# Kernel tuning notes

Measured on AMD Instinct MI355X. Metric: run time of the kernel, lower is better.

## Reference

```python
import jax, jax.numpy as jnp
import numpy as np

B, IN_F, OUT_F, H = 2048, 512, 512, 8
D = OUT_F // H  # head_dim = 64


def setup_inputs() -> dict:
    key = jax.random.key(0)
    ks = jax.random.split(key, 4)
    x = jax.random.normal(ks[0], (B, IN_F), dtype=jnp.float32)
    # learned params (per init_kwargs): nn.Linear(IN_F, OUT_F) and attention vector a
    W_w = jax.random.normal(ks[1], (OUT_F, IN_F), dtype=jnp.float32) * (1.0 / np.sqrt(IN_F))
    W_b = jnp.zeros((OUT_F,), dtype=jnp.float32)
    a = jax.random.normal(ks[2], (2 * D, 1), dtype=jnp.float32) * 0.1
    adj = jax.random.randint(ks[3], (B, B), 0, 2, dtype=jnp.int32)
    return {"x": x, "adj": adj, "W_w": W_w, "W_b": W_b, "a": a}


def reference(x, adj, W_w, W_b, a):
    Bn = x.shape[0]
    # h: [B, H, D]
    h = (x @ W_w.T + W_b).reshape(Bn, H, D)
    # decompose shared attention vector into src/dst halves (same for every head,
    # since torch code tiles a across heads via a.repeat(1, num_heads))
    a_src, a_dst = a[:D, 0], a[D:, 0]
    s_src = jnp.einsum('bhd,d->bh', h, a_src)  # [B, H] contribution of node i
    s_dst = jnp.einsum('bhd,d->bh', h, a_dst)  # [B, H] contribution of node j
    # e[i, j, h] = leakyrelu(h_i . a_src + h_j . a_dst)  -> [B, B, H]
    e = jax.nn.leaky_relu(s_src[:, None, :] + s_dst[None, :, :], negative_slope=0.2)
    e = jnp.where(adj[:, :, None] == 0, jnp.float32(-1e9), e)
    attn = jax.nn.softmax(e, axis=1)  # softmax over neighbors j (torch dim=1)
    # h_prime[i, h, :] = sum_j attn[i, j, h] * h[j, h, :]
    h_prime = jnp.einsum('ijh,jhd->ihd', attn, h).reshape(Bn, H * D)
    return jax.nn.elu(h_prime)
```

## Files before the change

### kernel.cpp

```cpp
#include <hip/hip_runtime.h>
#include <hip/hip_bf16.h>
#include <math.h>
#include <stdint.h>

#define BN 2048
#define KF 512
#define OF 512
#define NH 8
#define DD 64

typedef __attribute__((ext_vector_type(8))) short short8;
typedef __attribute__((ext_vector_type(4))) float f32x4;
typedef unsigned short ushortT;

static __device__ __forceinline__ ushortT bfcvt(float f) {
  __hip_bfloat16 h = __float2bfloat16(f);
  return *reinterpret_cast<ushortT*>(&h);
}
static __device__ __forceinline__ float bf2f(ushortT b) {
  return __uint_as_float(((unsigned)b) << 16);
}

#define SPLIT8(vsrc, dhi, dlo)                                        \
  {                                                                   \
    ushortT hi8[8], lo8[8];                                           \
    _Pragma("unroll") for (int i = 0; i < 8; ++i) {                   \
      hi8[i] = bfcvt((vsrc)[i]);                                      \
      lo8[i] = bfcvt((vsrc)[i] - bf2f(hi8[i]));                       \
    }                                                                 \
    (dhi) = *(const int4*)hi8;                                        \
    (dlo) = *(const int4*)lo8;                                        \
  }

__global__ __launch_bounds__(256, 2) void k_main(
    const float* __restrict__ x, const int* __restrict__ adj,
    const float* __restrict__ W, const float* __restrict__ Wb,
    const float* __restrict__ av,
    ushortT* __restrict__ hF, float* __restrict__ E12s, float* __restrict__ E12d,
    uint8_t* __restrict__ adjB) {
  __shared__ __align__(16) uint8_t smem[24576];
  __shared__ float sredS[2][32], sredD[2][32];

  const int t    = threadIdx.x;
  const int hh   = blockIdx.x;
  const int i0   = blockIdx.y * 32;
  const int b    = hh * 64 + blockIdx.y;
  const int lane = t & 63;
  const int wv   = t >> 6;
  const int mt   = wv & 1;
  const int nt   = wv >> 1;
  const int l15  = lane & 15;
  const int lq   = lane >> 4;

  {
    const int gtid = b * 256 + t;
#pragma unroll
    for (int it = 0; it < 4; ++it) {
      const int bidx = gtid + it * (512 * 256);
      const int4 v0 = *(const int4*)(adj + (size_t)bidx * 8);
      const int4 v1 = *(const int4*)(adj + (size_t)bidx * 8 + 4);
      unsigned m = (v0.x ? 1u : 0u) | (v0.y ? 2u : 0u) | (v0.z ? 4u : 0u) | (v0.w ? 8u : 0u)
                 | (v1.x ? 16u : 0u) | (v1.y ? 32u : 0u) | (v1.z ? 64u : 0u) | (v1.w ? 128u : 0u);
      adjB[bidx] = (uint8_t)m;
    }
  }

  ushortT* sAh = (ushortT*)smem;
  ushortT* sAl = sAh + 32 * 64;
  ushortT* sBh = sAl + 32 * 64;
  ushortT* sBl = sBh + 64 * 64;

  f32x4 acc[2] = {};
  const int srow = t >> 3, ss = t & 7;
  int4 aHi, aLo, bHi[2], bLo[2];

  {
    const float* xs = x + (size_t)(i0 + srow) * KF + ss * 8;
    float v[8];
    *(float4*)&v[0] = *(const float4*)xs;
    *(float4*)&v[4] = *(const float4*)(xs + 4);
    SPLIT8(v, aHi, aLo)
#pragma unroll
    for (int rp = 0; rp < 2; ++rp) {
      const int S = t + rp * 256, rw = S >> 3, s2 = S & 7;
      const float* wsrc = W + (size_t)(hh * 64 + rw) * KF + s2 * 8;
      float wv8[8];
      *(float4*)&wv8[0] = *(const float4*)wsrc;
      *(float4*)&wv8[4] = *(const float4*)(wsrc + 4);
      SPLIT8(wv8, bHi[rp], bLo[rp])
    }
  }

  for (int k0 = 0; k0 < 8; ++k0) {
    __syncthreads();
    {
      const int offA = srow * 64 + ((ss ^ (srow & 7)) * 8);
      *(int4*)&sAh[offA] = aHi;
      *(int4*)&sAl[offA] = aLo;
#pragma unroll
      for (int rp = 0; rp < 2; ++rp) {
        const int S = t + rp * 256, rw = S >> 3, s2 = S & 7;
        const int offB = rw * 64 + ((s2 ^ (rw & 7)) * 8);
        *(int4*)&sBh[offB] = bHi[rp];
        *(int4*)&sBl[offB] = bLo[rp];
      }
    }
    __syncthreads();
    if (k0 < 7) {
      const int kc = (k0 + 1) * 64;
      const float* xs = x + (size_t)(i0 + srow) * KF + kc + ss * 8;
      float v[8];
      *(float4*)&v[0] = *(const float4*)xs;
      *(float4*)&v[4] = *(const float4*)(xs + 4);
      SPLIT8(v, aHi, aLo)
#pragma unroll
      for (int rp = 0; rp < 2; ++rp) {
        const int S = t + rp * 256, rw = S >> 3, s2 = S & 7;
        const float* wsrc = W + (size_t)(hh * 64 + rw) * KF + kc + s2 * 8;
        float wv8[8];
        *(float4*)&wv8[0] = *(const float4*)wsrc;
        *(float4*)&wv8[4] = *(const float4*)(wsrc + 4);
        SPLIT8(wv8, bHi[rp], bLo[rp])
      }
    }
#pragma unroll
    for (int kb = 0; kb < 2; ++kb) {
      const int sc = kb * 4 + lq;
      const int arow = mt * 16 + l15;
      const int offA = arow * 64 + ((sc ^ (arow & 7)) * 8);
      const short8 afh = *(const short8*)&sAh[offA];
      const short8 afl = *(const short8*)&sAl[offA];
      const int br0 = nt * 32 + l15;
      const int br1 = br0 + 16;
      const int offB0 = br0 * 64 + ((sc ^ (br0 & 7)) * 8);
      const int offB1 = br1 * 64 + ((sc ^ (br1 & 7)) * 8);
      const short8 bh0 = *(const short8*)&sBh[offB0];
      const short8 bl0 = *(const short8*)&sBl[offB0];
      const short8 bh1 = *(const short8*)&sBh[offB1];
      const short8 bl1 = *(const short8*)&sBl[offB1];
      acc[0] = __builtin_amdgcn_mfma_f32_16x16x32_bf16(afh, bh0, acc[0], 0, 0, 0);
      acc[1] = __builtin_amdgcn_mfma_f32_16x16x32_bf16(afh, bh1, acc[1], 0, 0, 0);
      acc[0] = __builtin_amdgcn_mfma_f32_16x16x32_bf16(afh, bl0, acc[0], 0, 0, 0);
      acc[1] = __builtin_amdgcn_mfma_f32_16x16x32_bf16(afh, bl1, acc[1], 0, 0, 0);
      acc[0] = __builtin_amdgcn_mfma_f32_16x16x32_bf16(afl, bh0, acc[0], 0, 0, 0);
      acc[1] = __builtin_amdgcn_mfma_f32_16x16x32_bf16(afl, bh1, acc[1], 0, 0, 0);
    }
  }

  __syncthreads();
  ushortT* ldsT = (ushortT*)smem;
  float bias2[2], asv[2], adv[2];
#pragma unroll
  for (int bb = 0; bb < 2; ++bb) {
    const int fl = nt * 32 + bb * 16 + l15;
    bias2[bb] = Wb[hh * 64 + fl];
    asv[bb] = av[fl];
    adv[bb] = av[DD + fl];
  }
#pragma unroll
  for (int p = 0; p < 4; ++p) {
    float vs = 0.f, vd = 0.f;
#pragma unroll
    for (int bb = 0; bb < 2; ++bb) {
      const float hv = acc[bb][p] + bias2[bb];
      const ushortT hu = bfcvt(hv);
      vs = fmaf(hv, asv[bb], vs);
      vd = fmaf(hv, adv[bb], vd);
      ldsT[(nt * 32 + bb * 16 + l15) * 40 + mt * 16 + lq * 4 + p] = hu;
    }
    vs += __shfl_xor(vs, 1); vs += __shfl_xor(vs, 2);
    vs += __shfl_xor(vs, 4); vs += __shfl_xor(vs, 8);
    vd += __shfl_xor(vd, 1); vd += __shfl_xor(vd, 2);
    vd += __shfl_xor(vd, 4); vd += __shfl_xor(vd, 8);
    if (l15 == 0) {
      sredS[nt][mt * 16 + lq * 4 + p] = vs;
      sredD[nt][mt * 16 + lq * 4 + p] = vd;
    }
  }
  __syncthreads();
  if (t < 32) {
    const float s1 = sredS[0][t] + sredS[1][t];
    const float s2 = sredD[0][t] + sredD[1][t];
    const size_t gi = (size_t)hh * BN + i0 + t;
    float2 sv; sv.x = __expf(s1); sv.y = __expf(0.2f * s1);
    float2 dv; dv.x = __expf(s2); dv.y = __expf(0.2f * s2);
    *(float2*)&E12s[gi * 2] = sv;
    *(float2*)&E12d[gi * 2] = dv;
  }
  {
    const int n = t >> 6, ln = t & 63;
    const int4 v = *(const int4*)&ldsT[(n * 16 + (ln & 15)) * 40 + ((ln >> 4) * 8)];
    const size_t chunk = (((size_t)hh * 64 + blockIdx.y) * 4 + n) * 64 + ln;
    *(int4*)&hF[chunk * 8] = v;
  }
}

__global__ __launch_bounds__(512, 4) void k_attn(
    const ushortT* __restrict__ hF, const uint8_t* __restrict__ adjB,
    const float* __restrict__ E12s, const float* __restrict__ E12d,
    float* __restrict__ out) {
  __shared__ __align__(16) float e12[BN * 2];
  __shared__ __align__(16) float cbuf[4][2 * 16 * 68];
  __shared__ uint8_t abits[32 * 272];
  __shared__ float denP[8][2][16];
  __shared__ unsigned mlut[4];

  const int t    = threadIdx.x;
  const int hh   = blockIdx.x;
  const int i0   = blockIdx.y * 32;
  const int lane = t & 63;
  const int wv   = t >> 6;
  const int l15  = lane & 15;
  const int lq   = lane >> 4;

  {
    const float4* g = (const float4*)(E12d + (size_t)hh * BN * 2);
    ((float4*)e12)[t]       = g[t];
    ((float4*)e12)[t + 512] = g[t + 512];
    const int r = t >> 4, pp = t & 15;
    *(int4*)(abits + r * 272 + pp * 16) =
        *(const int4*)(adjB + (size_t)(i0 + r) * 256 + pp * 16);
    if (t < 4) mlut[t] = (t & 1 ? 0x0000FFFFu : 0u) | (t & 2 ? 0xFFFF0000u : 0u);
  }

  const float2 eiA = *(const float2*)&E12s[2 * ((size_t)hh * BN + i0 + l15)];
  const float2 eiB = *(const float2*)&E12s[2 * ((size_t)hh * BN + i0 + 16 + l15)];

  f32x4 acc0[4] = {};
  f32x4 acc1[4] = {};
  f32x4 accd0 = {0.f, 0.f, 0.f, 0.f}, accd1 = {0.f, 0.f, 0.f, 0.f};

  const short8 ones8 = {(short)0x3F80, (short)0x3F80, (short)0x3F80, (short)0x3F80,
                        (short)0x3F80, (short)0x3F80, (short)0x3F80, (short)0x3F80};

  const ushortT* hfb = hF + (size_t)hh * 64 * 4 * 64 * 8 + (size_t)lane * 8;

  __syncthreads();

  const int c0 = wv * 4;
  for (int c = c0; c < c0 + 4; ++c) {
    const uint64_t bits0 = *(const uint64_t*)(abits + l15 * 272 + c * 8);
    const uint64_t bits1 = *(const uint64_t*)(abits + (16 + l15) * 272 + c * 8);
#pragma unroll
    for (int kb = 0; kb < 2; ++kb) {
      const int jb = c * 2 + kb;
      const int j0 = jb * 32 + lq * 8;
      const float* ep = &e12[j0 * 2];
      const float4 r0 = *(const float4*)(ep);
      const float4 r1 = *(const float4*)(ep + 4);
      const float4 r2 = *(const float4*)(ep + 8);
      const float4 r3 = *(const float4*)(ep + 12);
      const unsigned bb0 = (unsigned)(bits0 >> ((kb * 4 + lq) * 8)) & 0xffu;
      const unsigned bb1 = (unsigned)(bits1 >> ((kb * 4 + lq) * 8)) & 0xffu;
      unsigned pk0[4], pk1[4];
#pragma unroll
      for (int q = 0; q < 4; ++q) {
        const float4 rq = (q == 0) ? r0 : (q == 1) ? r1 : (q == 2) ? r2 : r3;
        const float d1a = rq.x, d2a = rq.y, d1b = rq.z, d2b = rq.w;
        const unsigned m0 = mlut[(bb0 >> (2 * q)) & 3u];
        const unsigned m1 = mlut[(bb1 >> (2 * q)) & 3u];
        const float wa0 = fmaxf(eiA.x * d1a, eiA.y * d2a);
        const float wb0 = fmaxf(eiA.x * d1b, eiA.y * d2b);
        pk0[q] = (((unsigned)bfcvt(wa0)) | (((unsigned)bfcvt(wb0)) << 16)) & m0;
        const float wa1 = fmaxf(eiB.x * d1a, eiB.y * d2a);
        const float wb1 = fmaxf(eiB.x * d1b, eiB.y * d2b);
        pk1[q] = (((unsigned)bfcvt(wa1)) | (((unsigned)bfcvt(wb1)) << 16)) & m1;
      }
      const short8 af0 = *(const short8*)pk0;
      const short8 af1 = *(const short8*)pk1;
      const ushortT* fb = hfb + (size_t)(jb * 4) * 64 * 8;
#pragma unroll
      for (int n = 0; n < 4; ++n) {
        const short8 bf = *(const short8*)(fb + (size_t)n * 64 * 8);
        acc0[n] = __builtin_amdgcn_mfma_f32_16x16x32_bf16(af0, bf, acc0[n], 0, 0, 0);
        acc1[n] = __builtin_amdgcn_mfma_f32_16x16x32_bf16(af1, bf, acc1[n], 0, 0, 0);
      }
      accd0 = __builtin_amdgcn_mfma_f32_16x16x32_bf16(af0, ones8, accd0, 0, 0, 0);
      accd1 = __builtin_amdgcn_mfma_f32_16x16x32_bf16(af1, ones8, accd1, 0, 0, 0);
    }
  }

  if (l15 == 0) {
#pragma unroll
    for (int p = 0; p < 4; ++p) {
      denP[wv][0][lq * 4 + p] = accd0[p];
      denP[wv][1][lq * 4 + p] = accd1[p];
    }
  }

#define CWRITE(buf)                                                     \
  _Pragma("unroll") for (int n = 0; n < 4; ++n)                         \
  _Pragma("unroll") for (int p = 0; p < 4; ++p) {                       \
    (buf)[(lq * 4 + p) * 68 + n * 16 + l15]      = acc0[n][p];          \
    (buf)[(16 + lq * 4 + p) * 68 + n * 16 + l15] = acc1[n][p];          \
  }
#define CADD(buf)                                                       \
  _Pragma("unroll") for (int n = 0; n < 4; ++n)                         \
  _Pragma("unroll") for (int p = 0; p < 4; ++p) {                       \
    acc0[n][p] += (buf)[(lq * 4 + p) * 68 + n * 16 + l15];              \
    acc1[n][p] += (buf)[(16 + lq * 4 + p) * 68 + n * 16 + l15];         \
  }

  if (wv >= 4) { CWRITE(cbuf[wv - 4]) }
  __syncthreads();
  if (wv < 4) {
    CADD(cbuf[wv])
    if (wv >= 2) { CWRITE(cbuf[wv]) }
  }
  __syncthreads();
  if (wv < 2) {
    CADD(cbuf[wv + 2])
    if (wv == 1) { CWRITE(cbuf[1]) }
  }
  __syncthreads();
  if (wv == 0) {
    CADD(cbuf[1])
    float dfin0[4], dfin1[4];
#pragma unroll
    for (int p = 0; p < 4; ++p) {
      const int row = lq * 4 + p;
      float d0 = 0.f, d1s = 0.f;
#pragma unroll
      for (int w = 0; w < 8; ++w) { d0 += denP[w][0][row]; d1s += denP[w][1][row]; }
      dfin0[p] = 1.f / d0;
      dfin1[p] = 1.f / d1s;
    }
#pragma unroll
    for (int n = 0; n < 4; ++n)
#pragma unroll
      for (int p = 0; p < 4; ++p) {
        float v0 = acc0[n][p] * dfin0[p];
        float v1 = acc1[n][p] * dfin1[p];
        v0 = v0 > 0.f ? v0 : expm1f(v0);
        v1 = v1 > 0.f ? v1 : expm1f(v1);
        out[(size_t)(i0 + lq * 4 + p) * OF + hh * 64 + n * 16 + l15] = v0;
        out[(size_t)(i0 + 16 + lq * 4 + p) * OF + hh * 64 + n * 16 + l15] = v1;
      }
  }
#undef CWRITE
#undef CADD
}

extern "C" void kernel_launch(void* const* d_in, const int* in_sizes, int n_in,
                              void* d_out, int out_size, void* d_ws, size_t ws_size,
                              hipStream_t stream) {
  const float* x  = (const float*)d_in[0];
  const int* adj  = (const int*)d_in[1];
  const float* Ww = (const float*)d_in[2];
  const float* Wb = (const float*)d_in[3];
  const float* a  = (const float*)d_in[4];
  float* outp = (float*)d_out;

  uint8_t* p = (uint8_t*)d_ws;
  ushortT* hF   = (ushortT*)(p + 0x000000);
  float*   E12d = (float*)  (p + 0x200000);
  float*   E12s = (float*)  (p + 0x220000);
  uint8_t* adjB =            p + 0x240000;

  k_main<<<dim3(NH, BN / 32), 256, 0, stream>>>(x, adj, Ww, Wb, a, hF, E12s, E12d, adjB);
  k_attn<<<dim3(NH, BN / 32), 512, 0, stream>>>(hF, adjB, E12s, E12d, outp);
}
```

Measured before the change: 34.34 us.

## Fully unroll attention loop with double-buffered B loads and packed bf16 conversion

Fully unrolls the eight per-wave j-blocks and double-buffers the global hF fragment loads, so the next block's B operands are requested while the current block's MFMAs run. Adjacency bits are loaded once per wave as uint4 words. The shared-memory mask lookup table is replaced by per-element selects, and bf16 packing uses the v_cvt_pk_bf16_f32 instruction. The aim is to hide global load latency and cut LDS and ALU work, at the cost of more registers, which may reduce occupancy.

Result: faster. 33.06 us, median of 2 (-3.7%).

```diff
diff --git a/kernel.cpp b/kernel.cpp
--- a/kernel.cpp
+++ b/kernel.cpp
@@ -203,7 +203,6 @@
   __shared__ __align__(16) float cbuf[4][2 * 16 * 68];
   __shared__ uint8_t abits[32 * 272];
   __shared__ float denP[8][2][16];
-  __shared__ unsigned mlut[4];
 
   const int t    = threadIdx.x;
   const int hh   = blockIdx.x;
@@ -220,65 +219,84 @@
     const int r = t >> 4, pp = t & 15;
     *(int4*)(abits + r * 272 + pp * 16) =
         *(const int4*)(adjB + (size_t)(i0 + r) * 256 + pp * 16);
-    if (t < 4) mlut[t] = (t & 1 ? 0x0000FFFFu : 0u) | (t & 2 ? 0xFFFF0000u : 0u);
   }
 
   const float2 eiA = *(const float2*)&E12s[2 * ((size_t)hh * BN + i0 + l15)];
   const float2 eiB = *(const float2*)&E12s[2 * ((size_t)hh * BN + i0 + 16 + l15)];
 
-  f32x4 acc0[4] = {};
-  f32x4 acc1[4] = {};
-  f32x4 accd0 = {0.f, 0.f, 0.f, 0.f}, accd1 = {0.f, 0.f, 0.f, 0.f};
-
   const short8 ones8 = {(short)0x3F80, (short)0x3F80, (short)0x3F80, (short)0x3F80,
                         (short)0x3F80, (short)0x3F80, (short)0x3F80, (short)0x3F80};
 
-  const ushortT* hfb = hF + (size_t)hh * 64 * 4 * 64 * 8 + (size_t)lane * 8;
-
-  __syncthreads();
-
-  const int c0 = wv * 4;
-  for (int c = c0; c < c0 + 4; ++c) {
-    const uint64_t bits0 = *(const uint64_t*)(abits + l15 * 272 + c * 8);
-    const uint64_t bits1 = *(const uint64_t*)(abits + (16 + l15) * 272 + c * 8);
-#pragma unroll
-    for (int kb = 0; kb < 2; ++kb) {
-      const int jb = c * 2 + kb;
-      const int j0 = jb * 32 + lq * 8;
-      const float* ep = &e12[j0 * 2];
-      const float4 r0 = *(const float4*)(ep);
-      const float4 r1 = *(const float4*)(ep + 4);
-      const float4 r2 = *(const float4*)(ep + 8);
-      const float4 r3 = *(const float4*)(ep + 12);
-      const unsigned bb0 = (unsigned)(bits0 >> ((kb * 4 + lq) * 8)) & 0xffu;
-      const unsigned bb1 = (unsigned)(bits1 >> ((kb * 4 + lq) * 8)) & 0xffu;
-      unsigned pk0[4], pk1[4];
-#pragma unroll
-      for (int q = 0; q < 4; ++q) {
-        const float4 rq = (q == 0) ? r0 : (q == 1) ? r1 : (q == 2) ? r2 : r3;
-        const float d1a = rq.x, d2a = rq.y, d1b = rq.z, d2b = rq.w;
-        const unsigned m0 = mlut[(bb0 >> (2 * q)) & 3u];
-        const unsigned m1 = mlut[(bb1 >> (2 * q)) & 3u];
-        const float wa0 = fmaxf(eiA.x * d1a, eiA.y * d2a);
-        const float wb0 = fmaxf(eiA.x * d1b, eiA.y * d2b);
-        pk0[q] = (((unsigned)bfcvt(wa0)) | (((unsigned)bfcvt(wb0)) << 16)) & m0;
-        const float wa1 = fmaxf(eiB.x * d1a, eiB.y * d2a);
-        const float wb1 = fmaxf(eiB.x * d1b, eiB.y * d2b);
-        pk1[q] = (((unsigned)bfcvt(wa1)) | (((unsigned)bfcvt(wb1)) << 16)) & m1;
-      }
-      const short8 af0 = *(const short8*)pk0;
-      const short8 af1 = *(const short8*)pk1;
-      const ushortT* fb = hfb + (size_t)(jb * 4) * 64 * 8;
-#pragma unroll
-      for (int n = 0; n < 4; ++n) {
-        const short8 bf = *(const short8*)(fb + (size_t)n * 64 * 8);
-        acc0[n] = __builtin_amdgcn_mfma_f32_16x16x32_bf16(af0, bf, acc0[n], 0, 0, 0);
-        acc1[n] = __builtin_amdgcn_mfma_f32_16x16x32_bf16(af1, bf, acc1[n], 0, 0, 0);
-      }
-      accd0 = __builtin_amdgcn_mfma_f32_16x16x32_bf16(af0, ones8, accd0, 0, 0, 0);
-      accd1 = __builtin_amdgcn_mfma_f32_16x16x32_bf16(af1, ones8, accd1, 0, 0, 0);
-    }
-  }
+  const ushortT* hfb = hF + (size_t)hh * 131072 + (size_t)lane * 8;
+
+  __syncthreads();
+
+  const uint4 wA0 = *(const uint4*)(abits + l15 * 272 + wv * 32);
+  const uint4 wA1 = *(const uint4*)(abits + l15 * 272 + wv * 32 + 16);
+  const uint4 wB0 = *(const uint4*)(abits + (16 + l15) * 272 + wv * 32);
+  const uint4 wB1 = *(const uint4*)(abits + (16 + l15) * 272 + wv * 32 + 16);
+  const int lqs = lq * 8;
+
+  f32x4 acc0[4] = {}, acc1[4] = {};
+  f32x4 accd0 = {0.f, 0.f, 0.f, 0.f}, accd1 = {0.f, 0.f, 0.f, 0.f};
+
+  const int jb0 = wv * 8;
+  short8 bfA[4], bfB[4];
+  {
+    const ushortT* b0 = hfb + (size_t)(jb0 * 4) * 512;
+#pragma unroll
+    for (int n = 0; n < 4; ++n) bfA[n] = *(const short8*)(b0 + (size_t)n * 512);
+  }
+
+#define WSEL0(s) ((s)==0?wA0.x:(s)==1?wA0.y:(s)==2?wA0.z:(s)==3?wA0.w: \
+                  (s)==4?wA1.x:(s)==5?wA1.y:(s)==6?wA1.z:wA1.w)
+#define WSEL1(s) ((s)==0?wB0.x:(s)==1?wB0.y:(s)==2?wB0.z:(s)==3?wB0.w: \
+                  (s)==4?wB1.x:(s)==5?wB1.y:(s)==6?wB1.z:wB1.w)
+
+#define STEP(s, BCUR, BNXT)                                                        \
+  {                                                                                \
+    if ((s) < 7) {                                                                 \
+      const ushortT* bn = hfb + (size_t)((jb0 + (s) + 1) * 4) * 512;               \
+      _Pragma("unroll") for (int n = 0; n < 4; ++n)                                \
+        BNXT[n] = *(const short8*)(bn + (size_t)n * 512);                          \
+    }                                                                              \
+    const int j0 = (jb0 + (s)) * 32 + lq * 8;                                      \
+    const float* ep = &e12[j0 * 2];                                                \
+    const float4 r0 = *(const float4*)(ep);                                        \
+    const float4 r1 = *(const float4*)(ep + 4);                                    \
+    const float4 r2 = *(const float4*)(ep + 8);                                    \
+    const float4 r3 = *(const float4*)(ep + 12);                                   \
+    const unsigned bb0 = (WSEL0(s) >> lqs) & 0xffu;                                \
+    const unsigned bb1 = (WSEL1(s) >> lqs) & 0xffu;                                \
+    unsigned pk0[4], pk1[4];                                                       \
+    _Pragma("unroll") for (int q = 0; q < 4; ++q) {                                \
+      const float4 rq = (q == 0) ? r0 : (q == 1) ? r1 : (q == 2) ? r2 : r3;        \
+      float wa0 = fmaxf(eiA.x * rq.x, eiA.y * rq.y);                               \
+      float wb0 = fmaxf(eiA.x * rq.z, eiA.y * rq.w);                               \
+      float wa1 = fmaxf(eiB.x * rq.x, eiB.y * rq.y);                               \
+      float wb1 = fmaxf(eiB.x * rq.z, eiB.y * rq.w);                               \
+      wa0 = ((bb0 >> (2 * q)) & 1u) ? wa0 : 0.f;                                   \
+      wb0 = ((bb0 >> (2 * q + 1)) & 1u) ? wb0 : 0.f;                               \
+      wa1 = ((bb1 >> (2 * q)) & 1u) ? wa1 : 0.f;                                   \
+      wb1 = ((bb1 >> (2 * q + 1)) & 1u) ? wb1 : 0.f;                               \
+      asm("v_cvt_pk_bf16_f32 %0, %1, %2" : "=v"(pk0[q]) : "v"(wa0), "v"(wb0));     \
+      asm("v_cvt_pk_bf16_f32 %0, %1, %2" : "=v"(pk1[q]) : "v"(wa1), "v"(wb1));     \
+    }                                                                              \
+    const short8 af0 = *(const short8*)pk0;                                        \
+    const short8 af1 = *(const short8*)pk1;                                        \
+    _Pragma("unroll") for (int n = 0; n < 4; ++n) {                                \
+      acc0[n] = __builtin_amdgcn_mfma_f32_16x16x32_bf16(af0, BCUR[n], acc0[n], 0, 0, 0); \
+      acc1[n] = __builtin_amdgcn_mfma_f32_16x16x32_bf16(af1, BCUR[n], acc1[n], 0, 0, 0); \
+    }                                                                              \
+    accd0 = __builtin_amdgcn_mfma_f32_16x16x32_bf16(af0, ones8, accd0, 0, 0, 0);   \
+    accd1 = __builtin_amdgcn_mfma_f32_16x16x32_bf16(af1, ones8, accd1, 0, 0, 0);   \
+  }
+
+  STEP(0, bfA, bfB) STEP(1, bfB, bfA) STEP(2, bfA, bfB) STEP(3, bfB, bfA)
+  STEP(4, bfA, bfB) STEP(5, bfB, bfA) STEP(6, bfA, bfB) STEP(7, bfB, bfA)
+#undef STEP
+#undef WSEL0
+#undef WSEL1
 
   if (l15 == 0) {
 #pragma unroll
```
